# Performance work log

Hardware: AMD Instinct MI355X
Metric: run time of the kernel (lower is better)

## Reference

```python
import jax, jax.numpy as jnp
import numpy as np

B, D, H = 512, 512, 512  # batch, input dim, hidden dim


def setup_inputs() -> dict:
    key = jax.random.key(0)
    ks = jax.random.split(key, 7)
    s = 1.0 / np.sqrt(D)
    return {
        "x": jax.random.normal(ks[0], (B, D), jnp.float32),
        "W1": jax.random.normal(ks[1], (D, H), jnp.float32) * s,
        "b1": jax.random.normal(ks[2], (H,), jnp.float32) * 0.01,
        "W2": jax.random.normal(ks[3], (H, H), jnp.float32) * s,
        "b2": jax.random.normal(ks[4], (H,), jnp.float32) * 0.01,
        "w3": jax.random.normal(ks[5], (H,), jnp.float32) * s,
        "b3": jax.random.normal(ks[6], (1,), jnp.float32) * 0.01,
    }


def _per_sample(xi, W1, b1, W2, b2, w3, b3):
    # Sequential layers applied to one sample; per-sample scalar loss.
    h = jax.nn.relu(xi @ W1 + b1)
    h = jax.nn.relu(h @ W2 + b2)
    return h @ w3 + b3[0]


def reference(x, W1, b1, W2, b2, w3, b3):
    # Forward pass (vectorized over the batch) -> per-sample losses [B].
    h = jax.nn.relu(x @ W1 + b1)
    h = jax.nn.relu(h @ W2 + b2)
    output = h @ w3 + b3[0]  # [B]

    # _autogram: per-sample Jacobian w.r.t. all layer parameters with a seed
    # of ones (grad = ones_like(output)); gramian accumulates J @ J.T per
    # parameter block. jax.vmap(jax.grad) == torch.vmap(vjp) with scalar seed 1.
    grad_fn = jax.grad(_per_sample, argnums=(1, 2, 3, 4, 5, 6))
    grads = jax.vmap(grad_fn, in_axes=(0, None, None, None, None, None, None))(
        x, W1, b1, W2, b2, w3, b3
    )  # pytree of per-sample grads, each leaf [B, *param_shape]

    bsz = x.shape[0]
    gramian = jnp.zeros((bsz, bsz), x.dtype)
    for g in grads:  # fixed small number of parameter tensors (matches per-layer loop)
        J = g.reshape(bsz, -1)  # [B, n_params_block]
        gramian = gramian + J @ J.T
    return output, gramian
```

## Files before the change

### kernel.cpp

```cpp
#include <hip/hip_runtime.h>


#define NN 512

typedef __attribute__((ext_vector_type(8))) short v8s;
typedef __attribute__((ext_vector_type(4))) float v4f;

static __device__ __forceinline__ unsigned short f2bf(float f) {
    union { float f; unsigned u; } v; v.f = f;
    unsigned r = v.u + 0x7FFF + ((v.u >> 16) & 1);
    return (unsigned short)(r >> 16);
}
static __device__ __forceinline__ float bf2f(unsigned short h) {
    union { unsigned u; float f; } v; v.u = ((unsigned)h) << 16;
    return v.f;
}

__global__ __launch_bounds__(256) void prep(
    const float* __restrict__ x, const float* __restrict__ W1,
    const float* __restrict__ W2, const float* __restrict__ b3,
    unsigned short* __restrict__ xhi, unsigned short* __restrict__ xlo,
    unsigned short* __restrict__ W1th, unsigned short* __restrict__ W1tl,
    unsigned short* __restrict__ W2th, unsigned short* __restrict__ W2tl,
    unsigned short* __restrict__ W2b, float* __restrict__ out) {
    __shared__ float T[32][33];
    const int t = threadIdx.x;
    const int lr = t >> 3, lc = (t & 7) * 4;
    const int r0 = blockIdx.y * 32, c0 = blockIdx.x * 32;
    const int z = blockIdx.z;
    if (z == 2) {
        float4 v = *(const float4*)&x[(r0 + lr) * NN + c0 + lc];
        ushort4 hi, lo;
        hi.x = f2bf(v.x); lo.x = f2bf(v.x - bf2f(hi.x));
        hi.y = f2bf(v.y); lo.y = f2bf(v.y - bf2f(hi.y));
        hi.z = f2bf(v.z); lo.z = f2bf(v.z - bf2f(hi.z));
        hi.w = f2bf(v.w); lo.w = f2bf(v.w - bf2f(hi.w));
        *(ushort4*)&xhi[(r0 + lr) * NN + c0 + lc] = hi;
        *(ushort4*)&xlo[(r0 + lr) * NN + c0 + lc] = lo;
        if (blockIdx.x == 0 && t < 32) out[r0 + t] = b3[0];
        return;
    }
    const float* src = (z == 1) ? W2 : W1;
    float4 v = *(const float4*)&src[(r0 + lr) * NN + c0 + lc];
    if (z == 1) {
        ushort4 h;
        h.x = f2bf(v.x); h.y = f2bf(v.y); h.z = f2bf(v.z); h.w = f2bf(v.w);
        *(ushort4*)&W2b[(r0 + lr) * NN + c0 + lc] = h;
    }
    T[lr][lc + 0] = v.x; T[lr][lc + 1] = v.y;
    T[lr][lc + 2] = v.z; T[lr][lc + 3] = v.w;
    __syncthreads();
    unsigned short* dh = (z == 1) ? W2th : W1th;
    unsigned short* dl = (z == 1) ? W2tl : W1tl;
    float a0 = T[lc + 0][lr], a1 = T[lc + 1][lr];
    float a2 = T[lc + 2][lr], a3 = T[lc + 3][lr];
    ushort4 hi, lo;
    hi.x = f2bf(a0); lo.x = f2bf(a0 - bf2f(hi.x));
    hi.y = f2bf(a1); lo.y = f2bf(a1 - bf2f(hi.y));
    hi.z = f2bf(a2); lo.z = f2bf(a2 - bf2f(hi.z));
    hi.w = f2bf(a3); lo.w = f2bf(a3 - bf2f(hi.w));
    *(ushort4*)&dh[(c0 + lr) * NN + r0 + lc] = hi;
    *(ushort4*)&dl[(c0 + lr) * NN + r0 + lc] = lo;
}

__global__ __launch_bounds__(256) void fwd1(
    const unsigned short* __restrict__ Ahi, const unsigned short* __restrict__ Alo,
    const unsigned short* __restrict__ Bhi, const unsigned short* __restrict__ Blo,
    const float* __restrict__ bias,
    unsigned short* __restrict__ Chi, unsigned short* __restrict__ Clo) {
    const int t = threadIdx.x;
    const int wave = t >> 6, lane = t & 63;
    const int r = lane & 15, quad = lane >> 4;
    const int i0 = blockIdx.y * 32 + 16 * (wave >> 1);
    const int j0 = blockIdx.x * 32 + 16 * (wave & 1);
    const int ao = (i0 + r) * NN + quad * 8;
    const int bo = (j0 + r) * NN + quad * 8;
    v4f hh = {0.f, 0.f, 0.f, 0.f}, lh = hh, hl = hh;
    #pragma unroll
    for (int k0 = 0; k0 < NN; k0 += 32) {
        v8s ah = *(const v8s*)(Ahi + ao + k0);
        v8s al = *(const v8s*)(Alo + ao + k0);
        v8s bh = *(const v8s*)(Bhi + bo + k0);
        v8s bl = *(const v8s*)(Blo + bo + k0);
        hh = __builtin_amdgcn_mfma_f32_16x16x32_bf16(ah, bh, hh, 0, 0, 0);
        lh = __builtin_amdgcn_mfma_f32_16x16x32_bf16(al, bh, lh, 0, 0, 0);
        hl = __builtin_amdgcn_mfma_f32_16x16x32_bf16(ah, bl, hl, 0, 0, 0);
    }
    const float bj = bias[j0 + r];
    #pragma unroll
    for (int rr = 0; rr < 4; ++rr) {
        const int i = i0 + quad * 4 + rr, j = j0 + r;
        float zv = (hh[rr] + lh[rr]) + hl[rr] + bj;
        float h = zv > 0.f ? zv : 0.f;
        unsigned short hi = f2bf(h);
        Chi[i * NN + j] = hi;
        Clo[i * NN + j] = f2bf(h - bf2f(hi));
    }
}

__global__ __launch_bounds__(256) void fwd2(
    const unsigned short* __restrict__ Ahi, const unsigned short* __restrict__ Alo,
    const unsigned short* __restrict__ Bhi, const unsigned short* __restrict__ Blo,
    const float* __restrict__ b2, const float* __restrict__ w3,
    unsigned short* __restrict__ H2b, unsigned short* __restrict__ G2b,
    float* __restrict__ out) {
    const int t = threadIdx.x;
    const int wave = t >> 6, lane = t & 63;
    const int r = lane & 15, quad = lane >> 4;
    const int i0 = blockIdx.y * 32 + 16 * (wave >> 1);
    const int j0 = blockIdx.x * 32 + 16 * (wave & 1);
    const int ao = (i0 + r) * NN + quad * 8;
    const int bo = (j0 + r) * NN + quad * 8;
    v4f hh = {0.f, 0.f, 0.f, 0.f}, lh = hh, hl = hh;
    #pragma unroll
    for (int k0 = 0; k0 < NN; k0 += 32) {
        v8s ah = *(const v8s*)(Ahi + ao + k0);
        v8s al = *(const v8s*)(Alo + ao + k0);
        v8s bh = *(const v8s*)(Bhi + bo + k0);
        v8s bl = *(const v8s*)(Blo + bo + k0);
        hh = __builtin_amdgcn_mfma_f32_16x16x32_bf16(ah, bh, hh, 0, 0, 0);
        lh = __builtin_amdgcn_mfma_f32_16x16x32_bf16(al, bh, lh, 0, 0, 0);
        hl = __builtin_amdgcn_mfma_f32_16x16x32_bf16(ah, bl, hl, 0, 0, 0);
    }
    const float bj = b2[j0 + r];
    const float wj = w3[j0 + r];
    const unsigned short wjb = f2bf(wj);
    #pragma unroll
    for (int rr = 0; rr < 4; ++rr) {
        const int i = i0 + quad * 4 + rr, j = j0 + r;
        float zv = (hh[rr] + lh[rr]) + hl[rr] + bj;
        float h = zv > 0.f ? zv : 0.f;
        H2b[i * NN + j] = f2bf(h);
        G2b[i * NN + j] = (zv > 0.f) ? wjb : (unsigned short)0;
        float p = h * wj;
        p += __shfl_xor(p, 1, 64);
        p += __shfl_xor(p, 2, 64);
        p += __shfl_xor(p, 4, 64);
        p += __shfl_xor(p, 8, 64);
        if (r == 0) atomicAdd(&out[i], p);
    }
}

__global__ __launch_bounds__(256) void g1k(
    const unsigned short* __restrict__ G2b, const unsigned short* __restrict__ W2b,
    const unsigned short* __restrict__ H1b, unsigned short* __restrict__ G1b) {
    const int t = threadIdx.x;
    const int wave = t >> 6, lane = t & 63;
    const int r = lane & 15, quad = lane >> 4;
    const int i0 = blockIdx.y * 32 + 16 * (wave >> 1);
    const int c0 = blockIdx.x * 32 + 16 * (wave & 1);
    const unsigned short* arow = G2b + (i0 + r) * NN + quad * 8;
    const unsigned short* brow = W2b + (c0 + r) * NN + quad * 8;
    v4f acc = {0.f, 0.f, 0.f, 0.f};
    #pragma unroll
    for (int k0 = 0; k0 < NN; k0 += 32) {
        v8s a = *(const v8s*)(arow + k0);
        v8s b = *(const v8s*)(brow + k0);
        acc = __builtin_amdgcn_mfma_f32_16x16x32_bf16(a, b, acc, 0, 0, 0);
    }
    #pragma unroll
    for (int rr = 0; rr < 4; ++rr) {
        const int i = i0 + quad * 4 + rr;
        const int c = c0 + r;
        float v = (H1b[i * NN + c] != 0) ? acc[rr] : 0.f;
        G1b[i * NN + c] = f2bf(v);
    }
}

__global__ __launch_bounds__(256) void gramk(
    const unsigned short* __restrict__ Xb, const unsigned short* __restrict__ H1b,
    const unsigned short* __restrict__ G1b, const unsigned short* __restrict__ H2b,
    const unsigned short* __restrict__ G2b, float* __restrict__ gram) {
    const int t = threadIdx.x;
    const int wave = t >> 6, lane = t & 63;
    const int r = lane & 15, quad = lane >> 4;
    const int i0 = blockIdx.y * 32 + 16 * (wave >> 1);
    const int j0 = blockIdx.x * 32 + 16 * (wave & 1);
    const int ao = (i0 + r) * NN + quad * 8;
    const int bo = (j0 + r) * NN + quad * 8;
    v4f a0 = {0.f,0.f,0.f,0.f}, a1 = a0, a2 = a0, a3 = a0, a4 = a0;
    #pragma unroll
    for (int k0 = 0; k0 < NN; k0 += 32) {
        v8s xa = *(const v8s*)(Xb  + ao + k0), xb2 = *(const v8s*)(Xb  + bo + k0);
        v8s ha = *(const v8s*)(H1b + ao + k0), hb  = *(const v8s*)(H1b + bo + k0);
        v8s ga = *(const v8s*)(G1b + ao + k0), gb  = *(const v8s*)(G1b + bo + k0);
        v8s ua = *(const v8s*)(H2b + ao + k0), ub  = *(const v8s*)(H2b + bo + k0);
        v8s va = *(const v8s*)(G2b + ao + k0), vb  = *(const v8s*)(G2b + bo + k0);
        a0 = __builtin_amdgcn_mfma_f32_16x16x32_bf16(xa, xb2, a0, 0, 0, 0);
        a1 = __builtin_amdgcn_mfma_f32_16x16x32_bf16(ha, hb,  a1, 0, 0, 0);
        a2 = __builtin_amdgcn_mfma_f32_16x16x32_bf16(ga, gb,  a2, 0, 0, 0);
        a3 = __builtin_amdgcn_mfma_f32_16x16x32_bf16(ua, ub,  a3, 0, 0, 0);
        a4 = __builtin_amdgcn_mfma_f32_16x16x32_bf16(va, vb,  a4, 0, 0, 0);
    }
    #pragma unroll
    for (int rr = 0; rr < 4; ++rr) {
        const int i = i0 + quad * 4 + rr;
        const int j = j0 + r;
        float g = 1.f + a3[rr] + a4[rr] * (1.f + a1[rr]) + a2[rr] * (1.f + a0[rr]);
        gram[i * NN + j] = g;
    }
}

extern "C" void kernel_launch(void* const* d_in, const int* in_sizes, int n_in,
                              void* d_out, int out_size, void* d_ws, size_t ws_size,
                              hipStream_t stream) {
    const float* x  = (const float*)d_in[0];
    const float* W1 = (const float*)d_in[1];
    const float* b1 = (const float*)d_in[2];
    const float* W2 = (const float*)d_in[3];
    const float* b2 = (const float*)d_in[4];
    const float* w3 = (const float*)d_in[5];
    const float* b3 = (const float*)d_in[6];

    float* out  = (float*)d_out;
    float* gram = out + NN;

    unsigned short* p    = (unsigned short*)d_ws;
    unsigned short* xhi  = p;  p += NN * NN;
    unsigned short* xlo  = p;  p += NN * NN;
    unsigned short* W1th = p;  p += NN * NN;
    unsigned short* W1tl = p;  p += NN * NN;
    unsigned short* W2th = p;  p += NN * NN;
    unsigned short* W2tl = p;  p += NN * NN;
    unsigned short* W2b  = p;  p += NN * NN;
    unsigned short* H1b  = p;  p += NN * NN;
    unsigned short* H1lo = p;  p += NN * NN;
    unsigned short* H2b  = p;  p += NN * NN;
    unsigned short* G2b  = p;  p += NN * NN;
    unsigned short* G1b  = p;  p += NN * NN;

    dim3 blk(256);
    prep <<<dim3(16, 16, 3), blk, 0, stream>>>(x, W1, W2, b3, xhi, xlo,
                                               W1th, W1tl, W2th, W2tl, W2b, out);
    fwd1 <<<dim3(16, 16), blk, 0, stream>>>(xhi, xlo, W1th, W1tl, b1, H1b, H1lo);
    fwd2 <<<dim3(16, 16), blk, 0, stream>>>(H1b, H1lo, W2th, W2tl, b2, w3,
                                            H2b, G2b, out);
    g1k  <<<dim3(16, 16), blk, 0, stream>>>(G2b, W2b, H1b, G1b);
    gramk<<<dim3(16, 16), blk, 0, stream>>>(xhi, H1b, G1b, H2b, G2b, gram);
}
```

Baseline: 114.7 us.

## Fuse five kernels into one cooperative kernel with grid-wide syncs

Replaces the prep, fwd1, fwd2, g1k and gram launches with one cooperative kernel of 256 blocks that runs every stage in sequence, separated by grid.sync(). The goal is to remove the launch overhead and inter-kernel gaps between five small launches. In exchange it adds the cost of grid barriers, and the prep stage now does x, W1 and W2 conversion serially within each block instead of over a z-dimension of 3 blocks. The out initialisation now uses atomicExch, which must finish before the later atomicAdd, and the grid sync guarantees that ordering.

```diff
diff --git a/kernel.cpp b/kernel.cpp
--- a/kernel.cpp
+++ b/kernel.cpp
@@ -1,4 +1,7 @@
 #include <hip/hip_runtime.h>
+#include <hip/hip_cooperative_groups.h>
+
+namespace cg = cooperative_groups;
 
 
 #define NN 512
@@ -16,19 +19,35 @@
     return v.f;
 }
 
-__global__ __launch_bounds__(256) void prep(
+__global__ __launch_bounds__(256, 1) void fused(
     const float* __restrict__ x, const float* __restrict__ W1,
-    const float* __restrict__ W2, const float* __restrict__ b3,
-    unsigned short* __restrict__ xhi, unsigned short* __restrict__ xlo,
-    unsigned short* __restrict__ W1th, unsigned short* __restrict__ W1tl,
-    unsigned short* __restrict__ W2th, unsigned short* __restrict__ W2tl,
-    unsigned short* __restrict__ W2b, float* __restrict__ out) {
+    const float* __restrict__ b1, const float* __restrict__ W2,
+    const float* __restrict__ b2, const float* __restrict__ w3,
+    const float* __restrict__ b3, float* __restrict__ out,
+    float* __restrict__ gram, unsigned short* __restrict__ ws) {
+    unsigned short* xhi  = ws;
+    unsigned short* xlo  = xhi  + NN * NN;
+    unsigned short* W1th = xlo  + NN * NN;
+    unsigned short* W1tl = W1th + NN * NN;
+    unsigned short* W2th = W1tl + NN * NN;
+    unsigned short* W2tl = W2th + NN * NN;
+    unsigned short* W2b  = W2tl + NN * NN;
+    unsigned short* H1b  = W2b  + NN * NN;
+    unsigned short* H1lo = H1b  + NN * NN;
+    unsigned short* H2b  = H1lo + NN * NN;
+    unsigned short* G2b  = H2b  + NN * NN;
+    unsigned short* G1b  = G2b  + NN * NN;
+
+    cg::grid_group grid = cg::this_grid();
     __shared__ float T[32][33];
+
     const int t = threadIdx.x;
-    const int lr = t >> 3, lc = (t & 7) * 4;
-    const int r0 = blockIdx.y * 32, c0 = blockIdx.x * 32;
-    const int z = blockIdx.z;
-    if (z == 2) {
+    const int blk = blockIdx.x;
+    const int bx = blk & 15, by = blk >> 4;
+    const int r0 = by * 32, c0 = bx * 32;
+
+    {
+        const int lr = t >> 3, lc = (t & 7) * 4;
         float4 v = *(const float4*)&x[(r0 + lr) * NN + c0 + lc];
         ushort4 hi, lo;
         hi.x = f2bf(v.x); lo.x = f2bf(v.x - bf2f(hi.x));
@@ -37,167 +56,149 @@
         hi.w = f2bf(v.w); lo.w = f2bf(v.w - bf2f(hi.w));
         *(ushort4*)&xhi[(r0 + lr) * NN + c0 + lc] = hi;
         *(ushort4*)&xlo[(r0 + lr) * NN + c0 + lc] = lo;
-        if (blockIdx.x == 0 && t < 32) out[r0 + t] = b3[0];
-        return;
-    }
-    const float* src = (z == 1) ? W2 : W1;
-    float4 v = *(const float4*)&src[(r0 + lr) * NN + c0 + lc];
-    if (z == 1) {
-        ushort4 h;
-        h.x = f2bf(v.x); h.y = f2bf(v.y); h.z = f2bf(v.z); h.w = f2bf(v.w);
-        *(ushort4*)&W2b[(r0 + lr) * NN + c0 + lc] = h;
-    }
-    T[lr][lc + 0] = v.x; T[lr][lc + 1] = v.y;
-    T[lr][lc + 2] = v.z; T[lr][lc + 3] = v.w;
-    __syncthreads();
-    unsigned short* dh = (z == 1) ? W2th : W1th;
-    unsigned short* dl = (z == 1) ? W2tl : W1tl;
-    float a0 = T[lc + 0][lr], a1 = T[lc + 1][lr];
-    float a2 = T[lc + 2][lr], a3 = T[lc + 3][lr];
-    ushort4 hi, lo;
-    hi.x = f2bf(a0); lo.x = f2bf(a0 - bf2f(hi.x));
-    hi.y = f2bf(a1); lo.y = f2bf(a1 - bf2f(hi.y));
-    hi.z = f2bf(a2); lo.z = f2bf(a2 - bf2f(hi.z));
-    hi.w = f2bf(a3); lo.w = f2bf(a3 - bf2f(hi.w));
-    *(ushort4*)&dh[(c0 + lr) * NN + r0 + lc] = hi;
-    *(ushort4*)&dl[(c0 + lr) * NN + r0 + lc] = lo;
-}
-
-__global__ __launch_bounds__(256) void fwd1(
-    const unsigned short* __restrict__ Ahi, const unsigned short* __restrict__ Alo,
-    const unsigned short* __restrict__ Bhi, const unsigned short* __restrict__ Blo,
-    const float* __restrict__ bias,
-    unsigned short* __restrict__ Chi, unsigned short* __restrict__ Clo) {
-    const int t = threadIdx.x;
+        if (bx == 0 && t < 32) atomicExch(&out[r0 + t], b3[0]);
+
+        float4 w = *(const float4*)&W1[(r0 + lr) * NN + c0 + lc];
+        T[lr][lc + 0] = w.x; T[lr][lc + 1] = w.y;
+        T[lr][lc + 2] = w.z; T[lr][lc + 3] = w.w;
+        __syncthreads();
+        {
+            float a0 = T[lc + 0][lr], a1 = T[lc + 1][lr];
+            float a2 = T[lc + 2][lr], a3 = T[lc + 3][lr];
+            ushort4 h4, l4;
+            h4.x = f2bf(a0); l4.x = f2bf(a0 - bf2f(h4.x));
+            h4.y = f2bf(a1); l4.y = f2bf(a1 - bf2f(h4.y));
+            h4.z = f2bf(a2); l4.z = f2bf(a2 - bf2f(h4.z));
+            h4.w = f2bf(a3); l4.w = f2bf(a3 - bf2f(h4.w));
+            *(ushort4*)&W1th[(c0 + lr) * NN + r0 + lc] = h4;
+            *(ushort4*)&W1tl[(c0 + lr) * NN + r0 + lc] = l4;
+        }
+        __syncthreads();
+        float4 u = *(const float4*)&W2[(r0 + lr) * NN + c0 + lc];
+        ushort4 p4;
+        p4.x = f2bf(u.x); p4.y = f2bf(u.y); p4.z = f2bf(u.z); p4.w = f2bf(u.w);
+        *(ushort4*)&W2b[(r0 + lr) * NN + c0 + lc] = p4;
+        T[lr][lc + 0] = u.x; T[lr][lc + 1] = u.y;
+        T[lr][lc + 2] = u.z; T[lr][lc + 3] = u.w;
+        __syncthreads();
+        {
+            float a0 = T[lc + 0][lr], a1 = T[lc + 1][lr];
+            float a2 = T[lc + 2][lr], a3 = T[lc + 3][lr];
+            ushort4 h4, l4;
+            h4.x = f2bf(a0); l4.x = f2bf(a0 - bf2f(h4.x));
+            h4.y = f2bf(a1); l4.y = f2bf(a1 - bf2f(h4.y));
+            h4.z = f2bf(a2); l4.z = f2bf(a2 - bf2f(h4.z));
+            h4.w = f2bf(a3); l4.w = f2bf(a3 - bf2f(h4.w));
+            *(ushort4*)&W2th[(c0 + lr) * NN + r0 + lc] = h4;
+            *(ushort4*)&W2tl[(c0 + lr) * NN + r0 + lc] = l4;
+        }
+    }
+    grid.sync();
+
     const int wave = t >> 6, lane = t & 63;
     const int r = lane & 15, quad = lane >> 4;
-    const int i0 = blockIdx.y * 32 + 16 * (wave >> 1);
-    const int j0 = blockIdx.x * 32 + 16 * (wave & 1);
+    const int i0 = r0 + 16 * (wave >> 1);
+    const int j0 = c0 + 16 * (wave & 1);
     const int ao = (i0 + r) * NN + quad * 8;
     const int bo = (j0 + r) * NN + quad * 8;
-    v4f hh = {0.f, 0.f, 0.f, 0.f}, lh = hh, hl = hh;
-    #pragma unroll
-    for (int k0 = 0; k0 < NN; k0 += 32) {
-        v8s ah = *(const v8s*)(Ahi + ao + k0);
-        v8s al = *(const v8s*)(Alo + ao + k0);
-        v8s bh = *(const v8s*)(Bhi + bo + k0);
-        v8s bl = *(const v8s*)(Blo + bo + k0);
-        hh = __builtin_amdgcn_mfma_f32_16x16x32_bf16(ah, bh, hh, 0, 0, 0);
-        lh = __builtin_amdgcn_mfma_f32_16x16x32_bf16(al, bh, lh, 0, 0, 0);
-        hl = __builtin_amdgcn_mfma_f32_16x16x32_bf16(ah, bl, hl, 0, 0, 0);
-    }
-    const float bj = bias[j0 + r];
-    #pragma unroll
-    for (int rr = 0; rr < 4; ++rr) {
-        const int i = i0 + quad * 4 + rr, j = j0 + r;
-        float zv = (hh[rr] + lh[rr]) + hl[rr] + bj;
-        float h = zv > 0.f ? zv : 0.f;
-        unsigned short hi = f2bf(h);
-        Chi[i * NN + j] = hi;
-        Clo[i * NN + j] = f2bf(h - bf2f(hi));
-    }
-}
-
-__global__ __launch_bounds__(256) void fwd2(
-    const unsigned short* __restrict__ Ahi, const unsigned short* __restrict__ Alo,
-    const unsigned short* __restrict__ Bhi, const unsigned short* __restrict__ Blo,
-    const float* __restrict__ b2, const float* __restrict__ w3,
-    unsigned short* __restrict__ H2b, unsigned short* __restrict__ G2b,
-    float* __restrict__ out) {
-    const int t = threadIdx.x;
-    const int wave = t >> 6, lane = t & 63;
-    const int r = lane & 15, quad = lane >> 4;
-    const int i0 = blockIdx.y * 32 + 16 * (wave >> 1);
-    const int j0 = blockIdx.x * 32 + 16 * (wave & 1);
-    const int ao = (i0 + r) * NN + quad * 8;
-    const int bo = (j0 + r) * NN + quad * 8;
-    v4f hh = {0.f, 0.f, 0.f, 0.f}, lh = hh, hl = hh;
-    #pragma unroll
-    for (int k0 = 0; k0 < NN; k0 += 32) {
-        v8s ah = *(const v8s*)(Ahi + ao + k0);
-        v8s al = *(const v8s*)(Alo + ao + k0);
-        v8s bh = *(const v8s*)(Bhi + bo + k0);
-        v8s bl = *(const v8s*)(Blo + bo + k0);
-        hh = __builtin_amdgcn_mfma_f32_16x16x32_bf16(ah, bh, hh, 0, 0, 0);
-        lh = __builtin_amdgcn_mfma_f32_16x16x32_bf16(al, bh, lh, 0, 0, 0);
-        hl = __builtin_amdgcn_mfma_f32_16x16x32_bf16(ah, bl, hl, 0, 0, 0);
-    }
-    const float bj = b2[j0 + r];
-    const float wj = w3[j0 + r];
-    const unsigned short wjb = f2bf(wj);
-    #pragma unroll
-    for (int rr = 0; rr < 4; ++rr) {
-        const int i = i0 + quad * 4 + rr, j = j0 + r;
-        float zv = (hh[rr] + lh[rr]) + hl[rr] + bj;
-        float h = zv > 0.f ? zv : 0.f;
-        H2b[i * NN + j] = f2bf(h);
-        G2b[i * NN + j] = (zv > 0.f) ? wjb : (unsigned short)0;
-        float p = h * wj;
-        p += __shfl_xor(p, 1, 64);
-        p += __shfl_xor(p, 2, 64);
-        p += __shfl_xor(p, 4, 64);
-        p += __shfl_xor(p, 8, 64);
-        if (r == 0) atomicAdd(&out[i], p);
-    }
-}
-
-__global__ __launch_bounds__(256) void g1k(
-    const unsigned short* __restrict__ G2b, const unsigned short* __restrict__ W2b,
-    const unsigned short* __restrict__ H1b, unsigned short* __restrict__ G1b) {
-    const int t = threadIdx.x;
-    const int wave = t >> 6, lane = t & 63;
-    const int r = lane & 15, quad = lane >> 4;
-    const int i0 = blockIdx.y * 32 + 16 * (wave >> 1);
-    const int c0 = blockIdx.x * 32 + 16 * (wave & 1);
-    const unsigned short* arow = G2b + (i0 + r) * NN + quad * 8;
-    const unsigned short* brow = W2b + (c0 + r) * NN + quad * 8;
-    v4f acc = {0.f, 0.f, 0.f, 0.f};
-    #pragma unroll
-    for (int k0 = 0; k0 < NN; k0 += 32) {
-        v8s a = *(const v8s*)(arow + k0);
-        v8s b = *(const v8s*)(brow + k0);
-        acc = __builtin_amdgcn_mfma_f32_16x16x32_bf16(a, b, acc, 0, 0, 0);
-    }
-    #pragma unroll
-    for (int rr = 0; rr < 4; ++rr) {
-        const int i = i0 + quad * 4 + rr;
-        const int c = c0 + r;
-        float v = (H1b[i * NN + c] != 0) ? acc[rr] : 0.f;
-        G1b[i * NN + c] = f2bf(v);
-    }
-}
-
-__global__ __launch_bounds__(256) void gramk(
-    const unsigned short* __restrict__ Xb, const unsigned short* __restrict__ H1b,
-    const unsigned short* __restrict__ G1b, const unsigned short* __restrict__ H2b,
-    const unsigned short* __restrict__ G2b, float* __restrict__ gram) {
-    const int t = threadIdx.x;
-    const int wave = t >> 6, lane = t & 63;
-    const int r = lane & 15, quad = lane >> 4;
-    const int i0 = blockIdx.y * 32 + 16 * (wave >> 1);
-    const int j0 = blockIdx.x * 32 + 16 * (wave & 1);
-    const int ao = (i0 + r) * NN + quad * 8;
-    const int bo = (j0 + r) * NN + quad * 8;
-    v4f a0 = {0.f,0.f,0.f,0.f}, a1 = a0, a2 = a0, a3 = a0, a4 = a0;
-    #pragma unroll
-    for (int k0 = 0; k0 < NN; k0 += 32) {
-        v8s xa = *(const v8s*)(Xb  + ao + k0), xb2 = *(const v8s*)(Xb  + bo + k0);
-        v8s ha = *(const v8s*)(H1b + ao + k0), hb  = *(const v8s*)(H1b + bo + k0);
-        v8s ga = *(const v8s*)(G1b + ao + k0), gb  = *(const v8s*)(G1b + bo + k0);
-        v8s ua = *(const v8s*)(H2b + ao + k0), ub  = *(const v8s*)(H2b + bo + k0);
-        v8s va = *(const v8s*)(G2b + ao + k0), vb  = *(const v8s*)(G2b + bo + k0);
-        a0 = __builtin_amdgcn_mfma_f32_16x16x32_bf16(xa, xb2, a0, 0, 0, 0);
-        a1 = __builtin_amdgcn_mfma_f32_16x16x32_bf16(ha, hb,  a1, 0, 0, 0);
-        a2 = __builtin_amdgcn_mfma_f32_16x16x32_bf16(ga, gb,  a2, 0, 0, 0);
-        a3 = __builtin_amdgcn_mfma_f32_16x16x32_bf16(ua, ub,  a3, 0, 0, 0);
-        a4 = __builtin_amdgcn_mfma_f32_16x16x32_bf16(va, vb,  a4, 0, 0, 0);
-    }
-    #pragma unroll
-    for (int rr = 0; rr < 4; ++rr) {
-        const int i = i0 + quad * 4 + rr;
-        const int j = j0 + r;
-        float g = 1.f + a3[rr] + a4[rr] * (1.f + a1[rr]) + a2[rr] * (1.f + a0[rr]);
-        gram[i * NN + j] = g;
+
+    {
+        v4f hh = {0.f, 0.f, 0.f, 0.f}, lh = hh, hl = hh;
+        #pragma unroll
+        for (int k0 = 0; k0 < NN; k0 += 32) {
+            v8s ah = *(const v8s*)(xhi  + ao + k0);
+            v8s al = *(const v8s*)(xlo  + ao + k0);
+            v8s bh = *(const v8s*)(W1th + bo + k0);
+            v8s bl = *(const v8s*)(W1tl + bo + k0);
+            hh = __builtin_amdgcn_mfma_f32_16x16x32_bf16(ah, bh, hh, 0, 0, 0);
+            lh = __builtin_amdgcn_mfma_f32_16x16x32_bf16(al, bh, lh, 0, 0, 0);
+            hl = __builtin_amdgcn_mfma_f32_16x16x32_bf16(ah, bl, hl, 0, 0, 0);
+        }
+        const float bj = b1[j0 + r];
+        #pragma unroll
+        for (int rr = 0; rr < 4; ++rr) {
+            const int i = i0 + quad * 4 + rr, j = j0 + r;
+            float zv = (hh[rr] + lh[rr]) + hl[rr] + bj;
+            float h = zv > 0.f ? zv : 0.f;
+            unsigned short hi = f2bf(h);
+            H1b[i * NN + j]  = hi;
+            H1lo[i * NN + j] = f2bf(h - bf2f(hi));
+        }
+    }
+    grid.sync();
+
+    {
+        v4f hh = {0.f, 0.f, 0.f, 0.f}, lh = hh, hl = hh;
+        #pragma unroll
+        for (int k0 = 0; k0 < NN; k0 += 32) {
+            v8s ah = *(const v8s*)(H1b  + ao + k0);
+            v8s al = *(const v8s*)(H1lo + ao + k0);
+            v8s bh = *(const v8s*)(W2th + bo + k0);
+            v8s bl = *(const v8s*)(W2tl + bo + k0);
+            hh = __builtin_amdgcn_mfma_f32_16x16x32_bf16(ah, bh, hh, 0, 0, 0);
+            lh = __builtin_amdgcn_mfma_f32_16x16x32_bf16(al, bh, lh, 0, 0, 0);
+            hl = __builtin_amdgcn_mfma_f32_16x16x32_bf16(ah, bl, hl, 0, 0, 0);
+        }
+        const float bj = b2[j0 + r];
+        const float wj = w3[j0 + r];
+        const unsigned short wjb = f2bf(wj);
+        #pragma unroll
+        for (int rr = 0; rr < 4; ++rr) {
+            const int i = i0 + quad * 4 + rr, j = j0 + r;
+            float zv = (hh[rr] + lh[rr]) + hl[rr] + bj;
+            float h = zv > 0.f ? zv : 0.f;
+            H2b[i * NN + j] = f2bf(h);
+            G2b[i * NN + j] = (zv > 0.f) ? wjb : (unsigned short)0;
+            float p = h * wj;
+            p += __shfl_xor(p, 1, 64);
+            p += __shfl_xor(p, 2, 64);
+            p += __shfl_xor(p, 4, 64);
+            p += __shfl_xor(p, 8, 64);
+            if (r == 0) atomicAdd(&out[i], p);
+        }
+    }
+    grid.sync();
+
+    {
+        v4f acc = {0.f, 0.f, 0.f, 0.f};
+        #pragma unroll
+        for (int k0 = 0; k0 < NN; k0 += 32) {
+            v8s a = *(const v8s*)(G2b + ao + k0);
+            v8s b = *(const v8s*)(W2b + bo + k0);
+            acc = __builtin_amdgcn_mfma_f32_16x16x32_bf16(a, b, acc, 0, 0, 0);
+        }
+        #pragma unroll
+        for (int rr = 0; rr < 4; ++rr) {
+            const int i = i0 + quad * 4 + rr;
+            const int c = j0 + r;
+            float v = (H1b[i * NN + c] != 0) ? acc[rr] : 0.f;
+            G1b[i * NN + c] = f2bf(v);
+        }
+    }
+    grid.sync();
+
+    {
+        v4f a0 = {0.f,0.f,0.f,0.f}, a1 = a0, a2 = a0, a3 = a0, a4 = a0;
+        #pragma unroll
+        for (int k0 = 0; k0 < NN; k0 += 32) {
+            v8s xa = *(const v8s*)(xhi + ao + k0), xb2 = *(const v8s*)(xhi + bo + k0);
+            v8s ha = *(const v8s*)(H1b + ao + k0), hb  = *(const v8s*)(H1b + bo + k0);
+            v8s ga = *(const v8s*)(G1b + ao + k0), gb  = *(const v8s*)(G1b + bo + k0);
+            v8s ua = *(const v8s*)(H2b + ao + k0), ub  = *(const v8s*)(H2b + bo + k0);
+            v8s va = *(const v8s*)(G2b + ao + k0), vb  = *(const v8s*)(G2b + bo + k0);
+            a0 = __builtin_amdgcn_mfma_f32_16x16x32_bf16(xa, xb2, a0, 0, 0, 0);
+            a1 = __builtin_amdgcn_mfma_f32_16x16x32_bf16(ha, hb,  a1, 0, 0, 0);
+            a2 = __builtin_amdgcn_mfma_f32_16x16x32_bf16(ga, gb,  a2, 0, 0, 0);
+            a3 = __builtin_amdgcn_mfma_f32_16x16x32_bf16(ua, ub,  a3, 0, 0, 0);
+            a4 = __builtin_amdgcn_mfma_f32_16x16x32_bf16(va, vb,  a4, 0, 0, 0);
+        }
+        #pragma unroll
+        for (int rr = 0; rr < 4; ++rr) {
+            const int i = i0 + quad * 4 + rr;
+            const int j = j0 + r;
+            float g = 1.f + a3[rr] + a4[rr] * (1.f + a1[rr]) + a2[rr] * (1.f + a0[rr]);
+            gram[i * NN + j] = g;
+        }
     }
 }
 
@@ -214,27 +215,10 @@
 
     float* out  = (float*)d_out;
     float* gram = out + NN;
-
-    unsigned short* p    = (unsigned short*)d_ws;
-    unsigned short* xhi  = p;  p += NN * NN;
-    unsigned short* xlo  = p;  p += NN * NN;
-    unsigned short* W1th = p;  p += NN * NN;
-    unsigned short* W1tl = p;  p += NN * NN;
-    unsigned short* W2th = p;  p += NN * NN;
-    unsigned short* W2tl = p;  p += NN * NN;
-    unsigned short* W2b  = p;  p += NN * NN;
-    unsigned short* H1b  = p;  p += NN * NN;
-    unsigned short* H1lo = p;  p += NN * NN;
-    unsigned short* H2b  = p;  p += NN * NN;
-    unsigned short* G2b  = p;  p += NN * NN;
-    unsigned short* G1b  = p;  p += NN * NN;
-
-    dim3 blk(256);
-    prep <<<dim3(16, 16, 3), blk, 0, stream>>>(x, W1, W2, b3, xhi, xlo,
-                                               W1th, W1tl, W2th, W2tl, W2b, out);
-    fwd1 <<<dim3(16, 16), blk, 0, stream>>>(xhi, xlo, W1th, W1tl, b1, H1b, H1lo);
-    fwd2 <<<dim3(16, 16), blk, 0, stream>>>(H1b, H1lo, W2th, W2tl, b2, w3,
-                                            H2b, G2b, out);
-    g1k  <<<dim3(16, 16), blk, 0, stream>>>(G2b, W2b, H1b, G1b);
-    gramk<<<dim3(16, 16), blk, 0, stream>>>(xhi, H1b, G1b, H2b, G2b, gram);
-}
+    unsigned short* ws = (unsigned short*)d_ws;
+
+    void* kargs[] = {(void*)&x, (void*)&W1, (void*)&b1, (void*)&W2, (void*)&b2,
+                     (void*)&w3, (void*)&b3, (void*)&out, (void*)&gram, (void*)&ws};
+    hipLaunchCooperativeKernel(reinterpret_cast<void*>(fused), dim3(256),
+                               dim3(256), kargs, 0, stream);
+}
```

New measurement: 238.2 us. +107.7%, slower.

## Split K across waves in all GEMM kernels with LDS reduction

Applied to the files above, without the earlier changes.

Each block now computes a single 16x16 output tile, and its four waves each take a quarter of the K dimension (128 each). Partial accumulators are combined through shared memory, and wave 0 runs the epilogue. The grid grows from 256 to 1024 blocks, which gives more parallelism across the CUs and a shorter serial MFMA chain per wave. In exchange it adds LDS traffic, a barrier and an idle epilogue for three of the four waves, and it loses the operand reuse the old 32x32 block tiles had.

```diff
diff --git a/kernel.cpp b/kernel.cpp
--- a/kernel.cpp
+++ b/kernel.cpp
@@ -63,21 +63,22 @@
     *(ushort4*)&dl[(c0 + lr) * NN + r0 + lc] = lo;
 }
 
-__global__ __launch_bounds__(256) void fwd1(
+
+__global__ __launch_bounds__(256, 4) void fwd1(
     const unsigned short* __restrict__ Ahi, const unsigned short* __restrict__ Alo,
     const unsigned short* __restrict__ Bhi, const unsigned short* __restrict__ Blo,
     const float* __restrict__ bias,
     unsigned short* __restrict__ Chi, unsigned short* __restrict__ Clo) {
-    const int t = threadIdx.x;
-    const int wave = t >> 6, lane = t & 63;
-    const int r = lane & 15, quad = lane >> 4;
-    const int i0 = blockIdx.y * 32 + 16 * (wave >> 1);
-    const int j0 = blockIdx.x * 32 + 16 * (wave & 1);
-    const int ao = (i0 + r) * NN + quad * 8;
-    const int bo = (j0 + r) * NN + quad * 8;
+    __shared__ v4f red[3][64];
+    const int t = threadIdx.x, wave = t >> 6, lane = t & 63;
+    const int r = lane & 15, quad = lane >> 4;
+    const int i0 = (blockIdx.x >> 5) * 16, j0 = (blockIdx.x & 31) * 16;
+    const int kw = wave * 128;
+    const int ao = (i0 + r) * NN + kw + quad * 8;
+    const int bo = (j0 + r) * NN + kw + quad * 8;
     v4f hh = {0.f, 0.f, 0.f, 0.f}, lh = hh, hl = hh;
     #pragma unroll
-    for (int k0 = 0; k0 < NN; k0 += 32) {
+    for (int k0 = 0; k0 < 128; k0 += 32) {
         v8s ah = *(const v8s*)(Ahi + ao + k0);
         v8s al = *(const v8s*)(Alo + ao + k0);
         v8s bh = *(const v8s*)(Bhi + bo + k0);
@@ -86,34 +87,40 @@
         lh = __builtin_amdgcn_mfma_f32_16x16x32_bf16(al, bh, lh, 0, 0, 0);
         hl = __builtin_amdgcn_mfma_f32_16x16x32_bf16(ah, bl, hl, 0, 0, 0);
     }
-    const float bj = bias[j0 + r];
-    #pragma unroll
-    for (int rr = 0; rr < 4; ++rr) {
-        const int i = i0 + quad * 4 + rr, j = j0 + r;
-        float zv = (hh[rr] + lh[rr]) + hl[rr] + bj;
-        float h = zv > 0.f ? zv : 0.f;
-        unsigned short hi = f2bf(h);
-        Chi[i * NN + j] = hi;
-        Clo[i * NN + j] = f2bf(h - bf2f(hi));
-    }
-}
-
-__global__ __launch_bounds__(256) void fwd2(
+    v4f z = (hh + lh) + hl;
+    if (wave) red[wave - 1][lane] = z;
+    __syncthreads();
+    if (wave == 0) {
+        z += red[0][lane]; z += red[1][lane]; z += red[2][lane];
+        const float bj = bias[j0 + r];
+        #pragma unroll
+        for (int rr = 0; rr < 4; ++rr) {
+            const int i = i0 + quad * 4 + rr, j = j0 + r;
+            float zv = z[rr] + bj;
+            float h = zv > 0.f ? zv : 0.f;
+            unsigned short hi = f2bf(h);
+            Chi[i * NN + j] = hi;
+            Clo[i * NN + j] = f2bf(h - bf2f(hi));
+        }
+    }
+}
+
+__global__ __launch_bounds__(256, 4) void fwd2(
     const unsigned short* __restrict__ Ahi, const unsigned short* __restrict__ Alo,
     const unsigned short* __restrict__ Bhi, const unsigned short* __restrict__ Blo,
     const float* __restrict__ b2, const float* __restrict__ w3,
     unsigned short* __restrict__ H2b, unsigned short* __restrict__ G2b,
     float* __restrict__ out) {
-    const int t = threadIdx.x;
-    const int wave = t >> 6, lane = t & 63;
-    const int r = lane & 15, quad = lane >> 4;
-    const int i0 = blockIdx.y * 32 + 16 * (wave >> 1);
-    const int j0 = blockIdx.x * 32 + 16 * (wave & 1);
-    const int ao = (i0 + r) * NN + quad * 8;
-    const int bo = (j0 + r) * NN + quad * 8;
+    __shared__ v4f red[3][64];
+    const int t = threadIdx.x, wave = t >> 6, lane = t & 63;
+    const int r = lane & 15, quad = lane >> 4;
+    const int i0 = (blockIdx.x >> 5) * 16, j0 = (blockIdx.x & 31) * 16;
+    const int kw = wave * 128;
+    const int ao = (i0 + r) * NN + kw + quad * 8;
+    const int bo = (j0 + r) * NN + kw + quad * 8;
     v4f hh = {0.f, 0.f, 0.f, 0.f}, lh = hh, hl = hh;
     #pragma unroll
-    for (int k0 = 0; k0 < NN; k0 += 32) {
+    for (int k0 = 0; k0 < 128; k0 += 32) {
         v8s ah = *(const v8s*)(Ahi + ao + k0);
         v8s al = *(const v8s*)(Alo + ao + k0);
         v8s bh = *(const v8s*)(Bhi + bo + k0);
@@ -122,65 +129,76 @@
         lh = __builtin_amdgcn_mfma_f32_16x16x32_bf16(al, bh, lh, 0, 0, 0);
         hl = __builtin_amdgcn_mfma_f32_16x16x32_bf16(ah, bl, hl, 0, 0, 0);
     }
-    const float bj = b2[j0 + r];
-    const float wj = w3[j0 + r];
-    const unsigned short wjb = f2bf(wj);
-    #pragma unroll
-    for (int rr = 0; rr < 4; ++rr) {
-        const int i = i0 + quad * 4 + rr, j = j0 + r;
-        float zv = (hh[rr] + lh[rr]) + hl[rr] + bj;
-        float h = zv > 0.f ? zv : 0.f;
-        H2b[i * NN + j] = f2bf(h);
-        G2b[i * NN + j] = (zv > 0.f) ? wjb : (unsigned short)0;
-        float p = h * wj;
-        p += __shfl_xor(p, 1, 64);
-        p += __shfl_xor(p, 2, 64);
-        p += __shfl_xor(p, 4, 64);
-        p += __shfl_xor(p, 8, 64);
-        if (r == 0) atomicAdd(&out[i], p);
-    }
-}
-
-__global__ __launch_bounds__(256) void g1k(
+    v4f z = (hh + lh) + hl;
+    if (wave) red[wave - 1][lane] = z;
+    __syncthreads();
+    if (wave == 0) {
+        z += red[0][lane]; z += red[1][lane]; z += red[2][lane];
+        const float bj = b2[j0 + r];
+        const float wj = w3[j0 + r];
+        const unsigned short wjb = f2bf(wj);
+        #pragma unroll
+        for (int rr = 0; rr < 4; ++rr) {
+            const int i = i0 + quad * 4 + rr, j = j0 + r;
+            float zv = z[rr] + bj;
+            float h = zv > 0.f ? zv : 0.f;
+            H2b[i * NN + j] = f2bf(h);
+            G2b[i * NN + j] = (zv > 0.f) ? wjb : (unsigned short)0;
+            float p = h * wj;
+            p += __shfl_xor(p, 1, 64);
+            p += __shfl_xor(p, 2, 64);
+            p += __shfl_xor(p, 4, 64);
+            p += __shfl_xor(p, 8, 64);
+            if (r == 0) atomicAdd(&out[i], p);
+        }
+    }
+}
+
+__global__ __launch_bounds__(256, 4) void g1k(
     const unsigned short* __restrict__ G2b, const unsigned short* __restrict__ W2b,
     const unsigned short* __restrict__ H1b, unsigned short* __restrict__ G1b) {
-    const int t = threadIdx.x;
-    const int wave = t >> 6, lane = t & 63;
-    const int r = lane & 15, quad = lane >> 4;
-    const int i0 = blockIdx.y * 32 + 16 * (wave >> 1);
-    const int c0 = blockIdx.x * 32 + 16 * (wave & 1);
-    const unsigned short* arow = G2b + (i0 + r) * NN + quad * 8;
-    const unsigned short* brow = W2b + (c0 + r) * NN + quad * 8;
+    __shared__ v4f red[3][64];
+    const int t = threadIdx.x, wave = t >> 6, lane = t & 63;
+    const int r = lane & 15, quad = lane >> 4;
+    const int i0 = (blockIdx.x >> 5) * 16, c0 = (blockIdx.x & 31) * 16;
+    const int kw = wave * 128;
+    const unsigned short* arow = G2b + (i0 + r) * NN + kw + quad * 8;
+    const unsigned short* brow = W2b + (c0 + r) * NN + kw + quad * 8;
     v4f acc = {0.f, 0.f, 0.f, 0.f};
     #pragma unroll
-    for (int k0 = 0; k0 < NN; k0 += 32) {
+    for (int k0 = 0; k0 < 128; k0 += 32) {
         v8s a = *(const v8s*)(arow + k0);
         v8s b = *(const v8s*)(brow + k0);
         acc = __builtin_amdgcn_mfma_f32_16x16x32_bf16(a, b, acc, 0, 0, 0);
     }
-    #pragma unroll
-    for (int rr = 0; rr < 4; ++rr) {
-        const int i = i0 + quad * 4 + rr;
-        const int c = c0 + r;
-        float v = (H1b[i * NN + c] != 0) ? acc[rr] : 0.f;
-        G1b[i * NN + c] = f2bf(v);
-    }
-}
-
-__global__ __launch_bounds__(256) void gramk(
+    if (wave) red[wave - 1][lane] = acc;
+    __syncthreads();
+    if (wave == 0) {
+        acc += red[0][lane]; acc += red[1][lane]; acc += red[2][lane];
+        #pragma unroll
+        for (int rr = 0; rr < 4; ++rr) {
+            const int i = i0 + quad * 4 + rr;
+            const int c = c0 + r;
+            float v = (H1b[i * NN + c] != 0) ? acc[rr] : 0.f;
+            G1b[i * NN + c] = f2bf(v);
+        }
+    }
+}
+
+__global__ __launch_bounds__(256, 4) void gramk(
     const unsigned short* __restrict__ Xb, const unsigned short* __restrict__ H1b,
     const unsigned short* __restrict__ G1b, const unsigned short* __restrict__ H2b,
     const unsigned short* __restrict__ G2b, float* __restrict__ gram) {
-    const int t = threadIdx.x;
-    const int wave = t >> 6, lane = t & 63;
-    const int r = lane & 15, quad = lane >> 4;
-    const int i0 = blockIdx.y * 32 + 16 * (wave >> 1);
-    const int j0 = blockIdx.x * 32 + 16 * (wave & 1);
-    const int ao = (i0 + r) * NN + quad * 8;
-    const int bo = (j0 + r) * NN + quad * 8;
+    __shared__ v4f red[3][5][64];
+    const int t = threadIdx.x, wave = t >> 6, lane = t & 63;
+    const int r = lane & 15, quad = lane >> 4;
+    const int i0 = (blockIdx.x >> 5) * 16, j0 = (blockIdx.x & 31) * 16;
+    const int kw = wave * 128;
+    const int ao = (i0 + r) * NN + kw + quad * 8;
+    const int bo = (j0 + r) * NN + kw + quad * 8;
     v4f a0 = {0.f,0.f,0.f,0.f}, a1 = a0, a2 = a0, a3 = a0, a4 = a0;
     #pragma unroll
-    for (int k0 = 0; k0 < NN; k0 += 32) {
+    for (int k0 = 0; k0 < 128; k0 += 32) {
         v8s xa = *(const v8s*)(Xb  + ao + k0), xb2 = *(const v8s*)(Xb  + bo + k0);
         v8s ha = *(const v8s*)(H1b + ao + k0), hb  = *(const v8s*)(H1b + bo + k0);
         v8s ga = *(const v8s*)(G1b + ao + k0), gb  = *(const v8s*)(G1b + bo + k0);
@@ -192,12 +210,26 @@
         a3 = __builtin_amdgcn_mfma_f32_16x16x32_bf16(ua, ub,  a3, 0, 0, 0);
         a4 = __builtin_amdgcn_mfma_f32_16x16x32_bf16(va, vb,  a4, 0, 0, 0);
     }
-    #pragma unroll
-    for (int rr = 0; rr < 4; ++rr) {
-        const int i = i0 + quad * 4 + rr;
-        const int j = j0 + r;
-        float g = 1.f + a3[rr] + a4[rr] * (1.f + a1[rr]) + a2[rr] * (1.f + a0[rr]);
-        gram[i * NN + j] = g;
+    if (wave) {
+        red[wave - 1][0][lane] = a0; red[wave - 1][1][lane] = a1;
+        red[wave - 1][2][lane] = a2; red[wave - 1][3][lane] = a3;
+        red[wave - 1][4][lane] = a4;
+    }
+    __syncthreads();
+    if (wave == 0) {
+        #pragma unroll
+        for (int w = 0; w < 3; ++w) {
+            a0 += red[w][0][lane]; a1 += red[w][1][lane];
+            a2 += red[w][2][lane]; a3 += red[w][3][lane];
+            a4 += red[w][4][lane];
+        }
+        #pragma unroll
+        for (int rr = 0; rr < 4; ++rr) {
+            const int i = i0 + quad * 4 + rr;
+            const int j = j0 + r;
+            float g = 1.f + a3[rr] + a4[rr] * (1.f + a1[rr]) + a2[rr] * (1.f + a0[rr]);
+            gram[i * NN + j] = g;
+        }
     }
 }
 
@@ -232,9 +264,9 @@
     dim3 blk(256);
     prep <<<dim3(16, 16, 3), blk, 0, stream>>>(x, W1, W2, b3, xhi, xlo,
                                                W1th, W1tl, W2th, W2tl, W2b, out);
-    fwd1 <<<dim3(16, 16), blk, 0, stream>>>(xhi, xlo, W1th, W1tl, b1, H1b, H1lo);
-    fwd2 <<<dim3(16, 16), blk, 0, stream>>>(H1b, H1lo, W2th, W2tl, b2, w3,
-                                            H2b, G2b, out);
-    g1k  <<<dim3(16, 16), blk, 0, stream>>>(G2b, W2b, H1b, G1b);
-    gramk<<<dim3(16, 16), blk, 0, stream>>>(xhi, H1b, G1b, H2b, G2b, gram);
-}
+    fwd1 <<<dim3(1024), blk, 0, stream>>>(xhi, xlo, W1th, W1tl, b1, H1b, H1lo);
+    fwd2 <<<dim3(1024), blk, 0, stream>>>(H1b, H1lo, W2th, W2tl, b2, w3,
+                                          H2b, G2b, out);
+    g1k  <<<dim3(1024), blk, 0, stream>>>(G2b, W2b, H1b, G1b);
+    gramk<<<dim3(1024), blk, 0, stream>>>(xhi, H1b, G1b, H2b, G2b, gram);
+}
```

Result: slower. 118.2 us (+3.0%).

## Fuse input prep into forward GEMMs with in-LDS weight transpose and split

Applied to the files above, without the earlier changes.

Removes the separate prep kernel. Each forward GEMM block now loads its 32-column slab of the fp32 weight, splits it into bf16 hi/lo, transposes it into LDS, and converts x on the fly in registers. This saves a launch and the global round trip through the transposed hi/lo buffers. In exchange every block repeats the conversion of a full 512x32 weight slab (16x redundant across row blocks), uses about 66KB of LDS per block, which limits occupancy, and relies on side-effect writes of xhi and W2b from a subset of blocks.

```diff
diff --git a/kernel.cpp b/kernel.cpp
--- a/kernel.cpp
+++ b/kernel.cpp
@@ -16,108 +16,124 @@
     return v.f;
 }
 
-__global__ __launch_bounds__(256) void prep(
+__global__ __launch_bounds__(256) void fwd1(
     const float* __restrict__ x, const float* __restrict__ W1,
-    const float* __restrict__ W2, const float* __restrict__ b3,
-    unsigned short* __restrict__ xhi, unsigned short* __restrict__ xlo,
-    unsigned short* __restrict__ W1th, unsigned short* __restrict__ W1tl,
-    unsigned short* __restrict__ W2th, unsigned short* __restrict__ W2tl,
-    unsigned short* __restrict__ W2b, float* __restrict__ out) {
-    __shared__ float T[32][33];
-    const int t = threadIdx.x;
-    const int lr = t >> 3, lc = (t & 7) * 4;
-    const int r0 = blockIdx.y * 32, c0 = blockIdx.x * 32;
-    const int z = blockIdx.z;
-    if (z == 2) {
-        float4 v = *(const float4*)&x[(r0 + lr) * NN + c0 + lc];
-        ushort4 hi, lo;
-        hi.x = f2bf(v.x); lo.x = f2bf(v.x - bf2f(hi.x));
-        hi.y = f2bf(v.y); lo.y = f2bf(v.y - bf2f(hi.y));
-        hi.z = f2bf(v.z); lo.z = f2bf(v.z - bf2f(hi.z));
-        hi.w = f2bf(v.w); lo.w = f2bf(v.w - bf2f(hi.w));
-        *(ushort4*)&xhi[(r0 + lr) * NN + c0 + lc] = hi;
-        *(ushort4*)&xlo[(r0 + lr) * NN + c0 + lc] = lo;
-        if (blockIdx.x == 0 && t < 32) out[r0 + t] = b3[0];
-        return;
-    }
-    const float* src = (z == 1) ? W2 : W1;
-    float4 v = *(const float4*)&src[(r0 + lr) * NN + c0 + lc];
-    if (z == 1) {
-        ushort4 h;
-        h.x = f2bf(v.x); h.y = f2bf(v.y); h.z = f2bf(v.z); h.w = f2bf(v.w);
-        *(ushort4*)&W2b[(r0 + lr) * NN + c0 + lc] = h;
-    }
-    T[lr][lc + 0] = v.x; T[lr][lc + 1] = v.y;
-    T[lr][lc + 2] = v.z; T[lr][lc + 3] = v.w;
+    const float* __restrict__ b1, const float* __restrict__ b3,
+    unsigned short* __restrict__ xhi_out,
+    unsigned short* __restrict__ H1b, unsigned short* __restrict__ H1lo,
+    float* __restrict__ out) {
+    __shared__ unsigned short Bh[32][520];
+    __shared__ unsigned short Bl[32][520];
+    const int t = threadIdx.x;
+    const int bx = blockIdx.x & 15, by = blockIdx.x >> 4;
+    const int i0b = by * 32, j0b = bx * 32;
+
+    {
+        const int c4 = (t & 7) * 4;
+        const int rb = t >> 3;
+        #pragma unroll
+        for (int rnd = 0; rnd < 16; ++rnd) {
+            const int row = rnd * 32 + rb;
+            float4 v = *(const float4*)&W1[row * NN + j0b + c4];
+            unsigned short h;
+            h = f2bf(v.x); Bh[c4 + 0][row] = h; Bl[c4 + 0][row] = f2bf(v.x - bf2f(h));
+            h = f2bf(v.y); Bh[c4 + 1][row] = h; Bl[c4 + 1][row] = f2bf(v.y - bf2f(h));
+            h = f2bf(v.z); Bh[c4 + 2][row] = h; Bl[c4 + 2][row] = f2bf(v.z - bf2f(h));
+            h = f2bf(v.w); Bh[c4 + 3][row] = h; Bl[c4 + 3][row] = f2bf(v.w - bf2f(h));
+        }
+    }
+    if (j0b == 0 && t < 32) out[i0b + t] = b3[0];
     __syncthreads();
-    unsigned short* dh = (z == 1) ? W2th : W1th;
-    unsigned short* dl = (z == 1) ? W2tl : W1tl;
-    float a0 = T[lc + 0][lr], a1 = T[lc + 1][lr];
-    float a2 = T[lc + 2][lr], a3 = T[lc + 3][lr];
-    ushort4 hi, lo;
-    hi.x = f2bf(a0); lo.x = f2bf(a0 - bf2f(hi.x));
-    hi.y = f2bf(a1); lo.y = f2bf(a1 - bf2f(hi.y));
-    hi.z = f2bf(a2); lo.z = f2bf(a2 - bf2f(hi.z));
-    hi.w = f2bf(a3); lo.w = f2bf(a3 - bf2f(hi.w));
-    *(ushort4*)&dh[(c0 + lr) * NN + r0 + lc] = hi;
-    *(ushort4*)&dl[(c0 + lr) * NN + r0 + lc] = lo;
-}
-
-__global__ __launch_bounds__(256) void fwd1(
-    const unsigned short* __restrict__ Ahi, const unsigned short* __restrict__ Alo,
-    const unsigned short* __restrict__ Bhi, const unsigned short* __restrict__ Blo,
-    const float* __restrict__ bias,
-    unsigned short* __restrict__ Chi, unsigned short* __restrict__ Clo) {
-    const int t = threadIdx.x;
-    const int wave = t >> 6, lane = t & 63;
-    const int r = lane & 15, quad = lane >> 4;
-    const int i0 = blockIdx.y * 32 + 16 * (wave >> 1);
-    const int j0 = blockIdx.x * 32 + 16 * (wave & 1);
-    const int ao = (i0 + r) * NN + quad * 8;
-    const int bo = (j0 + r) * NN + quad * 8;
+
+    const int wave = t >> 6, lane = t & 63;
+    const int r = lane & 15, quad = lane >> 4;
+    const int i0 = i0b + 16 * (wave >> 1);
+    const int j0 = j0b + 16 * (wave & 1);
+    const int jl = 16 * (wave & 1) + r;
+    const float* xrow = x + (i0 + r) * NN;
+    const bool dumpx = (j0b == 0) && ((wave & 1) == 0);
+
     v4f hh = {0.f, 0.f, 0.f, 0.f}, lh = hh, hl = hh;
     #pragma unroll
     for (int k0 = 0; k0 < NN; k0 += 32) {
-        v8s ah = *(const v8s*)(Ahi + ao + k0);
-        v8s al = *(const v8s*)(Alo + ao + k0);
-        v8s bh = *(const v8s*)(Bhi + bo + k0);
-        v8s bl = *(const v8s*)(Blo + bo + k0);
+        const int k = k0 + quad * 8;
+        float4 xa = *(const float4*)&xrow[k];
+        float4 xb = *(const float4*)&xrow[k + 4];
+        v8s ah, al;
+        {
+            float vv[8] = {xa.x, xa.y, xa.z, xa.w, xb.x, xb.y, xb.z, xb.w};
+            #pragma unroll
+            for (int e = 0; e < 8; ++e) {
+                unsigned short h = f2bf(vv[e]);
+                ((unsigned short*)&ah)[e] = h;
+                ((unsigned short*)&al)[e] = f2bf(vv[e] - bf2f(h));
+            }
+        }
+        v8s bh = *(const v8s*)&Bh[jl][k];
+        v8s bl = *(const v8s*)&Bl[jl][k];
         hh = __builtin_amdgcn_mfma_f32_16x16x32_bf16(ah, bh, hh, 0, 0, 0);
         lh = __builtin_amdgcn_mfma_f32_16x16x32_bf16(al, bh, lh, 0, 0, 0);
         hl = __builtin_amdgcn_mfma_f32_16x16x32_bf16(ah, bl, hl, 0, 0, 0);
-    }
-    const float bj = bias[j0 + r];
+        if (dumpx) *(v8s*)&xhi_out[(i0 + r) * NN + k] = ah;
+    }
+    const float bj = b1[j0 + r];
     #pragma unroll
     for (int rr = 0; rr < 4; ++rr) {
         const int i = i0 + quad * 4 + rr, j = j0 + r;
         float zv = (hh[rr] + lh[rr]) + hl[rr] + bj;
         float h = zv > 0.f ? zv : 0.f;
         unsigned short hi = f2bf(h);
-        Chi[i * NN + j] = hi;
-        Clo[i * NN + j] = f2bf(h - bf2f(hi));
+        H1b[i * NN + j]  = hi;
+        H1lo[i * NN + j] = f2bf(h - bf2f(hi));
     }
 }
 
 __global__ __launch_bounds__(256) void fwd2(
     const unsigned short* __restrict__ Ahi, const unsigned short* __restrict__ Alo,
-    const unsigned short* __restrict__ Bhi, const unsigned short* __restrict__ Blo,
-    const float* __restrict__ b2, const float* __restrict__ w3,
+    const float* __restrict__ W2, const float* __restrict__ b2,
+    const float* __restrict__ w3, unsigned short* __restrict__ W2b,
     unsigned short* __restrict__ H2b, unsigned short* __restrict__ G2b,
     float* __restrict__ out) {
-    const int t = threadIdx.x;
-    const int wave = t >> 6, lane = t & 63;
-    const int r = lane & 15, quad = lane >> 4;
-    const int i0 = blockIdx.y * 32 + 16 * (wave >> 1);
-    const int j0 = blockIdx.x * 32 + 16 * (wave & 1);
+    __shared__ unsigned short Bh[32][520];
+    __shared__ unsigned short Bl[32][520];
+    const int t = threadIdx.x;
+    const int bx = blockIdx.x & 15, by = blockIdx.x >> 4;
+    const int i0b = by * 32, j0b = bx * 32;
+
+    {
+        const int c4 = (t & 7) * 4;
+        const int rb = t >> 3;
+        const bool dumpw = (i0b == 0);
+        #pragma unroll
+        for (int rnd = 0; rnd < 16; ++rnd) {
+            const int row = rnd * 32 + rb;
+            float4 v = *(const float4*)&W2[row * NN + j0b + c4];
+            ushort4 h4;
+            h4.x = f2bf(v.x); h4.y = f2bf(v.y); h4.z = f2bf(v.z); h4.w = f2bf(v.w);
+            Bh[c4 + 0][row] = h4.x; Bl[c4 + 0][row] = f2bf(v.x - bf2f(h4.x));
+            Bh[c4 + 1][row] = h4.y; Bl[c4 + 1][row] = f2bf(v.y - bf2f(h4.y));
+            Bh[c4 + 2][row] = h4.z; Bl[c4 + 2][row] = f2bf(v.z - bf2f(h4.z));
+            Bh[c4 + 3][row] = h4.w; Bl[c4 + 3][row] = f2bf(v.w - bf2f(h4.w));
+            if (dumpw) *(ushort4*)&W2b[row * NN + j0b + c4] = h4;
+        }
+    }
+    __syncthreads();
+
+    const int wave = t >> 6, lane = t & 63;
+    const int r = lane & 15, quad = lane >> 4;
+    const int i0 = i0b + 16 * (wave >> 1);
+    const int j0 = j0b + 16 * (wave & 1);
+    const int jl = 16 * (wave & 1) + r;
     const int ao = (i0 + r) * NN + quad * 8;
-    const int bo = (j0 + r) * NN + quad * 8;
+
     v4f hh = {0.f, 0.f, 0.f, 0.f}, lh = hh, hl = hh;
     #pragma unroll
     for (int k0 = 0; k0 < NN; k0 += 32) {
+        const int k = k0 + quad * 8;
         v8s ah = *(const v8s*)(Ahi + ao + k0);
         v8s al = *(const v8s*)(Alo + ao + k0);
-        v8s bh = *(const v8s*)(Bhi + bo + k0);
-        v8s bl = *(const v8s*)(Blo + bo + k0);
+        v8s bh = *(const v8s*)&Bh[jl][k];
+        v8s bl = *(const v8s*)&Bl[jl][k];
         hh = __builtin_amdgcn_mfma_f32_16x16x32_bf16(ah, bh, hh, 0, 0, 0);
         lh = __builtin_amdgcn_mfma_f32_16x16x32_bf16(al, bh, lh, 0, 0, 0);
         hl = __builtin_amdgcn_mfma_f32_16x16x32_bf16(ah, bl, hl, 0, 0, 0);
@@ -217,24 +233,17 @@
 
     unsigned short* p    = (unsigned short*)d_ws;
     unsigned short* xhi  = p;  p += NN * NN;
-    unsigned short* xlo  = p;  p += NN * NN;
-    unsigned short* W1th = p;  p += NN * NN;
-    unsigned short* W1tl = p;  p += NN * NN;
-    unsigned short* W2th = p;  p += NN * NN;
-    unsigned short* W2tl = p;  p += NN * NN;
-    unsigned short* W2b  = p;  p += NN * NN;
     unsigned short* H1b  = p;  p += NN * NN;
     unsigned short* H1lo = p;  p += NN * NN;
     unsigned short* H2b  = p;  p += NN * NN;
     unsigned short* G2b  = p;  p += NN * NN;
     unsigned short* G1b  = p;  p += NN * NN;
+    unsigned short* W2b  = p;  p += NN * NN;
 
     dim3 blk(256);
-    prep <<<dim3(16, 16, 3), blk, 0, stream>>>(x, W1, W2, b3, xhi, xlo,
-                                               W1th, W1tl, W2th, W2tl, W2b, out);
-    fwd1 <<<dim3(16, 16), blk, 0, stream>>>(xhi, xlo, W1th, W1tl, b1, H1b, H1lo);
-    fwd2 <<<dim3(16, 16), blk, 0, stream>>>(H1b, H1lo, W2th, W2tl, b2, w3,
-                                            H2b, G2b, out);
+    fwd1 <<<dim3(256), blk, 0, stream>>>(x, W1, b1, b3, xhi, H1b, H1lo, out);
+    fwd2 <<<dim3(256), blk, 0, stream>>>(H1b, H1lo, W2, b2, w3, W2b,
+                                         H2b, G2b, out);
     g1k  <<<dim3(16, 16), blk, 0, stream>>>(G2b, W2b, H1b, G1b);
     gramk<<<dim3(16, 16), blk, 0, stream>>>(xhi, H1b, G1b, H2b, G2b, gram);
 }
```

Result: slower. 117.3 us (+2.3%).
